# Kernel tuning notes

Hardware: AMD Instinct MI355X
Metric: run time of the kernel (lower is better)

The kernel has to match this reference:

```python
import jax, jax.numpy as jnp
import numpy as np

B, T, I, H, O = 4096, 2048, 1, 2, 1

def setup_inputs() -> dict:
    key = jax.random.key(0)
    ks = jax.random.split(key, 7)
    s_ih = 1.0 / np.sqrt(H)
    return {
        "x": jax.random.normal(ks[0], (B, T, I), dtype=jnp.float32),
        "W_ih": jax.random.uniform(ks[1], (H, I), jnp.float32, -s_ih, s_ih),
        "W_hh": jax.random.uniform(ks[2], (H, H), jnp.float32, -s_ih, s_ih),
        "b_ih": jax.random.uniform(ks[3], (H,), jnp.float32, -s_ih, s_ih),
        "b_hh": jax.random.uniform(ks[4], (H,), jnp.float32, -s_ih, s_ih),
        "fc_w": jax.random.uniform(ks[5], (O, H + I), jnp.float32, -1.0/np.sqrt(H + I), 1.0/np.sqrt(H + I)),
        "fc_b": jax.random.uniform(ks[6], (O,), jnp.float32, -1.0/np.sqrt(H + I), 1.0/np.sqrt(H + I)),
    }

def reference(x, W_ih, W_hh, b_ih, b_hh, fc_w, fc_b):
    # Precompute input contribution for all timesteps: [B, T, H]
    xin = jnp.einsum('bti,hi->bth', x, W_ih) + b_ih + b_hh
    h0 = jnp.zeros((x.shape[0], W_hh.shape[0]), dtype=x.dtype)

    def step(h, xin_t):  # h: [B,H], xin_t: [B,H]
        h_new = jnp.tanh(xin_t + h @ W_hh.T)
        return h_new, h_new

    _, hen = jax.lax.scan(step, h0, jnp.swapaxes(xin, 0, 1))  # hen: [T,B,H]
    hen = jnp.swapaxes(hen, 0, 1)  # [B,T,H]
    cat = jnp.concatenate((x, hen), axis=2)  # [B,T,I+H]
    return jnp.einsum('btc,oc->bto', cat, fc_w) + fc_b
```

## Files before the change

kernel.cpp:

```cpp
#include <hip/hip_runtime.h>


typedef float f32x2 __attribute__((ext_vector_type(2)));
typedef float f32x4 __attribute__((ext_vector_type(4)));

constexpr int T_LEN   = 2048;
constexpr int CHUNK   = 32;
constexpr int WARM    = 32;
constexpr int WPB     = 4;
constexpr int THREADS = 256;
constexpr int OSPAN   = WPB * CHUNK;
constexpr int SPAN    = OSPAN + WARM;
constexpr int NCG     = T_LEN / OSPAN;

static __device__ inline float EXP2F(float x){ float r; asm("v_exp_f32 %0, %1":"=v"(r):"v"(x)); return r; }
static __device__ inline float RCPF(float x){ float r; asm("v_rcp_f32 %0, %1":"=v"(r):"v"(x)); return r; }
static __device__ inline f32x2 mk2(float a, float b){ f32x2 t; t.x=a; t.y=b; return t; }

#define PK_FMA_B0(d, s0, s1, s2)                                          \
    asm("v_pk_fma_f32 %0, %1, %2, %3 op_sel:[0,0,0] op_sel_hi:[0,1,1]"    \
        : "=v"(d) : "v"(s0), "v"(s1), "v"(s2))
#define PK_FMA_B1(d, s0, s1, s2)                                          \
    asm("v_pk_fma_f32 %0, %1, %2, %3 op_sel:[1,0,0] op_sel_hi:[1,1,1]"    \
        : "=v"(d) : "v"(s0), "v"(s1), "v"(s2))
#define PK_ADD(d, s0, s1)                                                 \
    asm("v_pk_add_f32 %0, %1, %2" : "=v"(d) : "v"(s0), "v"(s1))

#define PSTEP_CORE(bb)                                                    \
    do {                                                                  \
        f32x2 q_, p_, e_, d_;                                             \
        PK_FMA_B1(q_, rr, mm1, (bb));                                     \
        PK_FMA_B0(p_, rr, mm0, q_);                                       \
        e_.x = EXP2F(p_.x); e_.y = EXP2F(p_.y);                           \
        PK_ADD(d_, e_, ones);                                             \
        rr.x = RCPF(d_.x); rr.y = RCPF(d_.y);                             \
    } while (0)

#define WSTEP_LO(xp2) do { f32x2 b_; PK_FMA_B0(b_, (xp2), aa, cc); PSTEP_CORE(b_); } while (0)
#define WSTEP_HI(xp2) do { f32x2 b_; PK_FMA_B1(b_, (xp2), aa, cc); PSTEP_CORE(b_); } while (0)
#define OSTEP_LO(xp2, ok) do { WSTEP_LO(xp2); (ok) = fmaf(rr.y, g2, fmaf(rr.x, g1, fmaf((xp2).x, f0, fb))); } while (0)
#define OSTEP_HI(xp2, ok) do { WSTEP_HI(xp2); (ok) = fmaf(rr.y, g2, fmaf(rr.x, g1, fmaf((xp2).y, f0, fb))); } while (0)

__global__ __launch_bounds__(THREADS, 4) void rnn_pk(
    const float* __restrict__ x,
    const float* __restrict__ W_ih,
    const float* __restrict__ W_hh,
    const float* __restrict__ b_ih,
    const float* __restrict__ b_hh,
    const float* __restrict__ fc_w,
    const float* __restrict__ fc_b,
    float* __restrict__ out)
{
    __shared__ float lx[SPAN * 64];

    const int sg  = blockIdx.x >> 4;
    const int cg  = blockIdx.x & (NCG - 1);
    const int tid = threadIdx.x;

    const int tlo = cg ? cg * OSPAN - WARM : 0;
    const float* xg = x + (size_t)sg * 64 * T_LEN + tlo;

    if (cg != 0) {
        #pragma unroll
        for (int k = 0; k < 10; ++k) {
            int idx = k * THREADS + tid;
            int r = idx / 40, c = idx - r * 40;
            f32x4 v = *(const f32x4*)(xg + (size_t)r * T_LEN + c * 4);
            int A = c * 256 + (((r ^ c) & 63) << 1);
            *(f32x2*)&lx[A]       = mk2(v.x, v.y);
            *(f32x2*)&lx[A + 128] = mk2(v.z, v.w);
        }
    } else {
        #pragma unroll
        for (int k = 0; k < 8; ++k) {
            int idx = k * THREADS + tid;
            int r = idx >> 5, c = idx & 31;
            f32x4 v = *(const f32x4*)(xg + (size_t)r * T_LEN + c * 4);
            int A = c * 256 + (((r ^ c) & 63) << 1);
            *(f32x2*)&lx[A]       = mk2(v.x, v.y);
            *(f32x2*)&lx[A + 128] = mk2(v.z, v.w);
        }
    }
    __syncthreads();

    const float s = 2.0f * 1.44269504088896340736f;
    const float W00 = W_hh[0], W01 = W_hh[1], W10 = W_hh[2], W11 = W_hh[3];
    const f32x2 aa  = mk2(W_ih[0] * s, W_ih[1] * s);
    const f32x2 cc  = mk2((b_ih[0] + b_hh[0] + W00 + W01) * s,
                          (b_ih[1] + b_hh[1] + W10 + W11) * s);
    const f32x2 mm0 = mk2(-2.0f * s * W00, -2.0f * s * W10);
    const f32x2 mm1 = mk2(-2.0f * s * W01, -2.0f * s * W11);
    const f32x2 ones = mk2(1.0f, 1.0f);
    const float f0 = fc_w[0];
    const float g1 = -2.0f * fc_w[1], g2 = -2.0f * fc_w[2];
    const float fb = fc_b[0] + fc_w[1] + fc_w[2];

    const int w = tid >> 6, l = tid & 63;

    int q, warm_q;
    if (cg == 0) {
        int gt = w * CHUNK - WARM;
        if (gt < 0) gt = 0;
        q = gt >> 2;
        warm_q = (w * CHUNK - gt) >> 2;
    } else {
        q = (w * CHUNK) >> 2;
        warm_q = WARM >> 2;
    }

    f32x2 rr = mk2(0.5f, 0.5f);

    #pragma unroll 2
    for (int i = 0; i < warm_q; ++i, ++q) {
        int A = q * 256 + (((l ^ q) & 63) << 1);
        f32x2 xa = *(const f32x2*)&lx[A];
        f32x2 xb = *(const f32x2*)&lx[A + 128];
        WSTEP_LO(xa); WSTEP_HI(xa); WSTEP_LO(xb); WSTEP_HI(xb);
    }

    f32x4 o0, o1, o2, o3, o4, o5, o6, o7;
#define OQ(oo)                                                            \
    do {                                                                  \
        int A = q * 256 + (((l ^ q) & 63) << 1);                          \
        f32x2 xa = *(const f32x2*)&lx[A];                                 \
        f32x2 xb = *(const f32x2*)&lx[A + 128];                           \
        OSTEP_LO(xa, oo.x); OSTEP_HI(xa, oo.y);                           \
        OSTEP_LO(xb, oo.z); OSTEP_HI(xb, oo.w);                           \
        ++q;                                                              \
    } while (0)
    OQ(o0); OQ(o1); OQ(o2); OQ(o3); OQ(o4); OQ(o5); OQ(o6); OQ(o7);

    __syncthreads();
#define OWR(oo, j)                                                        \
    do {                                                                  \
        int qo = w * 8 + (j);                                             \
        int A = qo * 256 + (((l ^ qo) & 63) << 1);                        \
        *(f32x2*)&lx[A]       = mk2((oo).x, (oo).y);                      \
        *(f32x2*)&lx[A + 128] = mk2((oo).z, (oo).w);                      \
    } while (0)
    OWR(o0, 0); OWR(o1, 1); OWR(o2, 2); OWR(o3, 3);
    OWR(o4, 4); OWR(o5, 5); OWR(o6, 6); OWR(o7, 7);
    __syncthreads();

    float* og = out + (size_t)sg * 64 * T_LEN + cg * OSPAN;
    #pragma unroll
    for (int k = 0; k < 8; ++k) {
        int idx = k * THREADS + tid;
        int r = idx >> 5, c = idx & 31;
        int A = c * 256 + (((r ^ c) & 63) << 1);
        f32x2 lo = *(const f32x2*)&lx[A];
        f32x2 hi = *(const f32x2*)&lx[A + 128];
        f32x4 v;
        v.x = lo.x; v.y = lo.y; v.z = hi.x; v.w = hi.y;
        __builtin_nontemporal_store(v, (f32x4*)(og + (size_t)r * T_LEN + c * 4));
    }
}

extern "C" void kernel_launch(void* const* d_in, const int* in_sizes, int n_in,
                              void* d_out, int out_size, void* d_ws, size_t ws_size,
                              hipStream_t stream) {
    const float* x    = (const float*)d_in[0];
    const float* W_ih = (const float*)d_in[1];
    const float* W_hh = (const float*)d_in[2];
    const float* b_ih = (const float*)d_in[3];
    const float* b_hh = (const float*)d_in[4];
    const float* fc_w = (const float*)d_in[5];
    const float* fc_b = (const float*)d_in[6];
    float* out = (float*)d_out;

    const int B = in_sizes[0] / T_LEN;

    dim3 block(THREADS);
    dim3 grid((B / 64) * NCG);
    rnn_pk<<<grid, block, 0, stream>>>(x, W_ih, W_hh, b_ih, b_hh,
                                       fc_w, fc_b, out);
}
```

Before: 19.13 us.

## Switch to one-wavefront blocks, each owning a 32-step chunk, removing barriers

Each block is now a single 64-lane wavefront that handles one 32-timestep chunk for 64 sequences, loading its own warm-up window and staging output through LDS. The three __syncthreads calls go away, since one wavefront needs no block barrier, and the grid becomes 4096 small blocks instead of 512 four-wave blocks. In exchange, every chunk after the first now reloads its 32-step warm-up input, whereas before the four waves in a block shared overlapping input. Each block also reserves 16 KB of LDS for a single wave, which may limit how many waves fit per CU.

```diff
diff --git a/kernel.cpp b/kernel.cpp
--- a/kernel.cpp
+++ b/kernel.cpp
@@ -4,14 +4,10 @@
 typedef float f32x2 __attribute__((ext_vector_type(2)));
 typedef float f32x4 __attribute__((ext_vector_type(4)));
 
-constexpr int T_LEN   = 2048;
-constexpr int CHUNK   = 32;
-constexpr int WARM    = 32;
-constexpr int WPB     = 4;
-constexpr int THREADS = 256;
-constexpr int OSPAN   = WPB * CHUNK;
-constexpr int SPAN    = OSPAN + WARM;
-constexpr int NCG     = T_LEN / OSPAN;
+constexpr int T_LEN  = 2048;
+constexpr int CHUNK  = 32;
+constexpr int WARM   = 32;
+constexpr int NCHUNK = T_LEN / CHUNK;
 
 static __device__ inline float EXP2F(float x){ float r; asm("v_exp_f32 %0, %1":"=v"(r):"v"(x)); return r; }
 static __device__ inline float RCPF(float x){ float r; asm("v_rcp_f32 %0, %1":"=v"(r):"v"(x)); return r; }
@@ -41,7 +37,7 @@
 #define OSTEP_LO(xp2, ok) do { WSTEP_LO(xp2); (ok) = fmaf(rr.y, g2, fmaf(rr.x, g1, fmaf((xp2).x, f0, fb))); } while (0)
 #define OSTEP_HI(xp2, ok) do { WSTEP_HI(xp2); (ok) = fmaf(rr.y, g2, fmaf(rr.x, g1, fmaf((xp2).y, f0, fb))); } while (0)
 
-__global__ __launch_bounds__(THREADS, 4) void rnn_pk(
+__global__ __launch_bounds__(64) void rnn_wave(
     const float* __restrict__ x,
     const float* __restrict__ W_ih,
     const float* __restrict__ W_hh,
@@ -51,108 +47,98 @@
     const float* __restrict__ fc_b,
     float* __restrict__ out)
 {
-    __shared__ float lx[SPAN * 64];
+    __shared__ float lx[4096];
 
-    const int sg  = blockIdx.x >> 4;
-    const int cg  = blockIdx.x & (NCG - 1);
-    const int tid = threadIdx.x;
+    const int l   = threadIdx.x;
+    const int wid = blockIdx.x;
+    const int sg  = wid >> 6;
+    const int c   = wid & (NCHUNK - 1);
 
-    const int tlo = cg ? cg * OSPAN - WARM : 0;
-    const float* xg = x + (size_t)sg * 64 * T_LEN + tlo;
+    const int t0 = c ? c * CHUNK - WARM : 0;
+    const int q0 = c ? (WARM >> 2) : 0;
 
-    if (cg != 0) {
+    const float* xg = x + (size_t)(sg * 64) * T_LEN + t0;
+
+    if (c) {
         #pragma unroll
-        for (int k = 0; k < 10; ++k) {
-            int idx = k * THREADS + tid;
-            int r = idx / 40, c = idx - r * 40;
-            f32x4 v = *(const f32x4*)(xg + (size_t)r * T_LEN + c * 4);
-            int A = c * 256 + (((r ^ c) & 63) << 1);
+        for (int k = 0; k < 16; ++k) {
+            int s = (l >> 4) + (k << 2);
+            int q = l & 15;
+            f32x4 v = *(const f32x4*)(xg + (size_t)s * T_LEN + (q << 2));
+            int A = q * 256 + (((s ^ q) & 63) << 1);
             *(f32x2*)&lx[A]       = mk2(v.x, v.y);
             *(f32x2*)&lx[A + 128] = mk2(v.z, v.w);
         }
     } else {
         #pragma unroll
         for (int k = 0; k < 8; ++k) {
-            int idx = k * THREADS + tid;
-            int r = idx >> 5, c = idx & 31;
-            f32x4 v = *(const f32x4*)(xg + (size_t)r * T_LEN + c * 4);
-            int A = c * 256 + (((r ^ c) & 63) << 1);
+            int s = (l >> 3) + (k << 3);
+            int q = l & 7;
+            f32x4 v = *(const f32x4*)(xg + (size_t)s * T_LEN + (q << 2));
+            int A = q * 256 + (((s ^ q) & 63) << 1);
             *(f32x2*)&lx[A]       = mk2(v.x, v.y);
             *(f32x2*)&lx[A + 128] = mk2(v.z, v.w);
         }
     }
-    __syncthreads();
 
-    const float s = 2.0f * 1.44269504088896340736f;
+    const float s2 = 2.0f * 1.44269504088896340736f;
     const float W00 = W_hh[0], W01 = W_hh[1], W10 = W_hh[2], W11 = W_hh[3];
-    const f32x2 aa  = mk2(W_ih[0] * s, W_ih[1] * s);
-    const f32x2 cc  = mk2((b_ih[0] + b_hh[0] + W00 + W01) * s,
-                          (b_ih[1] + b_hh[1] + W10 + W11) * s);
-    const f32x2 mm0 = mk2(-2.0f * s * W00, -2.0f * s * W10);
-    const f32x2 mm1 = mk2(-2.0f * s * W01, -2.0f * s * W11);
+    const f32x2 aa  = mk2(W_ih[0] * s2, W_ih[1] * s2);
+    const f32x2 cc  = mk2((b_ih[0] + b_hh[0] + W00 + W01) * s2,
+                          (b_ih[1] + b_hh[1] + W10 + W11) * s2);
+    const f32x2 mm0 = mk2(-2.0f * s2 * W00, -2.0f * s2 * W10);
+    const f32x2 mm1 = mk2(-2.0f * s2 * W01, -2.0f * s2 * W11);
     const f32x2 ones = mk2(1.0f, 1.0f);
     const float f0 = fc_w[0];
     const float g1 = -2.0f * fc_w[1], g2 = -2.0f * fc_w[2];
     const float fb = fc_b[0] + fc_w[1] + fc_w[2];
 
-    const int w = tid >> 6, l = tid & 63;
-
-    int q, warm_q;
-    if (cg == 0) {
-        int gt = w * CHUNK - WARM;
-        if (gt < 0) gt = 0;
-        q = gt >> 2;
-        warm_q = (w * CHUNK - gt) >> 2;
-    } else {
-        q = (w * CHUNK) >> 2;
-        warm_q = WARM >> 2;
-    }
-
     f32x2 rr = mk2(0.5f, 0.5f);
 
-    #pragma unroll 2
-    for (int i = 0; i < warm_q; ++i, ++q) {
-        int A = q * 256 + (((l ^ q) & 63) << 1);
-        f32x2 xa = *(const f32x2*)&lx[A];
-        f32x2 xb = *(const f32x2*)&lx[A + 128];
-        WSTEP_LO(xa); WSTEP_HI(xa); WSTEP_LO(xb); WSTEP_HI(xb);
+    if (c) {
+        #pragma unroll
+        for (int q = 0; q < 8; ++q) {
+            int A = q * 256 + (((l ^ q) & 63) << 1);
+            f32x2 xa = *(const f32x2*)&lx[A];
+            f32x2 xb = *(const f32x2*)&lx[A + 128];
+            WSTEP_LO(xa); WSTEP_HI(xa); WSTEP_LO(xb); WSTEP_HI(xb);
+        }
     }
 
     f32x4 o0, o1, o2, o3, o4, o5, o6, o7;
-#define OQ(oo)                                                            \
+#define OQ(oo, j)                                                         \
     do {                                                                  \
+        int q = q0 + (j);                                                 \
         int A = q * 256 + (((l ^ q) & 63) << 1);                          \
         f32x2 xa = *(const f32x2*)&lx[A];                                 \
         f32x2 xb = *(const f32x2*)&lx[A + 128];                           \
         OSTEP_LO(xa, oo.x); OSTEP_HI(xa, oo.y);                           \
         OSTEP_LO(xb, oo.z); OSTEP_HI(xb, oo.w);                           \
-        ++q;                                                              \
     } while (0)
-    OQ(o0); OQ(o1); OQ(o2); OQ(o3); OQ(o4); OQ(o5); OQ(o6); OQ(o7);
+    OQ(o0, 0); OQ(o1, 1); OQ(o2, 2); OQ(o3, 3);
+    OQ(o4, 4); OQ(o5, 5); OQ(o6, 6); OQ(o7, 7);
 
-    __syncthreads();
 #define OWR(oo, j)                                                        \
     do {                                                                  \
-        int qo = w * 8 + (j);                                             \
-        int A = qo * 256 + (((l ^ qo) & 63) << 1);                        \
+        int q = q0 + (j);                                                 \
+        int A = q * 256 + (((l ^ q) & 63) << 1);                          \
         *(f32x2*)&lx[A]       = mk2((oo).x, (oo).y);                      \
         *(f32x2*)&lx[A + 128] = mk2((oo).z, (oo).w);                      \
     } while (0)
     OWR(o0, 0); OWR(o1, 1); OWR(o2, 2); OWR(o3, 3);
     OWR(o4, 4); OWR(o5, 5); OWR(o6, 6); OWR(o7, 7);
-    __syncthreads();
 
-    float* og = out + (size_t)sg * 64 * T_LEN + cg * OSPAN;
+    float* og = out + (size_t)(sg * 64) * T_LEN + c * CHUNK;
     #pragma unroll
     for (int k = 0; k < 8; ++k) {
-        int idx = k * THREADS + tid;
-        int r = idx >> 5, c = idx & 31;
-        int A = c * 256 + (((r ^ c) & 63) << 1);
+        int s = (l >> 3) + (k << 3);
+        int j = l & 7;
+        int q = q0 + j;
+        int A = q * 256 + (((s ^ q) & 63) << 1);
         f32x2 lo = *(const f32x2*)&lx[A];
         f32x2 hi = *(const f32x2*)&lx[A + 128];
-        f32x4 v;
-        v.x = lo.x; v.y = lo.y; v.z = hi.x; v.w = hi.y;
-        __builtin_nontemporal_store(v, (f32x4*)(og + (size_t)r * T_LEN + c * 4));
+        f32x4 v; v.x = lo.x; v.y = lo.y; v.z = hi.x; v.w = hi.y;
+        __builtin_nontemporal_store(v, (f32x4*)(og + (size_t)s * T_LEN + (j << 2)));
     }
 }
 
@@ -170,8 +156,8 @@
 
     const int B = in_sizes[0] / T_LEN;
 
-    dim3 block(THREADS);
-    dim3 grid((B / 64) * NCG);
-    rnn_pk<<<grid, block, 0, stream>>>(x, W_ih, W_hh, b_ih, b_hh,
-                                       fc_w, fc_b, out);
+    dim3 block(64);
+    dim3 grid(B);
+    rnn_wave<<<grid, block, 0, stream>>>(x, W_ih, W_hh, b_ih, b_hh,
+                                         fc_w, fc_b, out);
 }
```

New measurement: 26.08 us. 1.36x slower.

## Process two time chunks per block with register prefetch of next chunk

Applied to the files above, without the earlier changes.

Each block now handles two consecutive time-chunk groups instead of one, halving the grid. While the first chunk's recurrence runs, the second chunk's x tile is loaded into registers, so its global load latency overlaps compute. A separate LDS output buffer lets the input tile be rewritten while outputs are staged. In exchange, launch bounds drop to 2 blocks per CU and there are half as many blocks, which reduces parallelism and increases register and LDS pressure.

```diff
diff --git a/kernel.cpp b/kernel.cpp
--- a/kernel.cpp
+++ b/kernel.cpp
@@ -12,6 +12,7 @@
 constexpr int OSPAN   = WPB * CHUNK;
 constexpr int SPAN    = OSPAN + WARM;
 constexpr int NCG     = T_LEN / OSPAN;
+constexpr int XQ      = SPAN / 4;
 
 static __device__ inline float EXP2F(float x){ float r; asm("v_exp_f32 %0, %1":"=v"(r):"v"(x)); return r; }
 static __device__ inline float RCPF(float x){ float r; asm("v_rcp_f32 %0, %1":"=v"(r):"v"(x)); return r; }
@@ -41,7 +42,77 @@
 #define OSTEP_LO(xp2, ok) do { WSTEP_LO(xp2); (ok) = fmaf(rr.y, g2, fmaf(rr.x, g1, fmaf((xp2).x, f0, fb))); } while (0)
 #define OSTEP_HI(xp2, ok) do { WSTEP_HI(xp2); (ok) = fmaf(rr.y, g2, fmaf(rr.x, g1, fmaf((xp2).y, f0, fb))); } while (0)
 
-__global__ __launch_bounds__(THREADS, 4) void rnn_pk(
+#define LOADX(dst, xgp)                                                   \
+    do {                                                                  \
+        _Pragma("unroll")                                                 \
+        for (int k = 0; k < 10; ++k) {                                    \
+            int idx = k * THREADS + tid;                                  \
+            int r_ = idx / XQ, c_ = idx - r_ * XQ;                        \
+            dst[k] = *(const f32x4*)((xgp) + (size_t)r_ * T_LEN + c_ * 4);\
+        }                                                                 \
+    } while (0)
+
+#define WRITEX(src)                                                       \
+    do {                                                                  \
+        _Pragma("unroll")                                                 \
+        for (int k = 0; k < 10; ++k) {                                    \
+            int idx = k * THREADS + tid;                                  \
+            int r_ = idx / XQ, c_ = idx - r_ * XQ;                        \
+            int A_ = c_ * 256 + (((r_ ^ c_) & 63) << 1);                  \
+            *(f32x2*)&lx[A_]       = mk2(src[k].x, src[k].y);             \
+            *(f32x2*)&lx[A_ + 128] = mk2(src[k].z, src[k].w);             \
+        }                                                                 \
+    } while (0)
+
+#define COMPUTE_OWR(cg)                                                   \
+    do {                                                                  \
+        int q, warm_q;                                                    \
+        if ((cg) == 0) {                                                  \
+            int gt = w * CHUNK - WARM; if (gt < 0) gt = 0;                \
+            q = gt >> 2; warm_q = (w * CHUNK - gt) >> 2;                  \
+        } else {                                                          \
+            q = (w * CHUNK) >> 2; warm_q = WARM >> 2;                     \
+        }                                                                 \
+        f32x2 rr = mk2(0.5f, 0.5f);                                       \
+        _Pragma("unroll 2")                                               \
+        for (int i = 0; i < warm_q; ++i, ++q) {                           \
+            int A_ = q * 256 + (((l ^ q) & 63) << 1);                     \
+            f32x2 xa_ = *(const f32x2*)&lx[A_];                           \
+            f32x2 xb_ = *(const f32x2*)&lx[A_ + 128];                     \
+            WSTEP_LO(xa_); WSTEP_HI(xa_); WSTEP_LO(xb_); WSTEP_HI(xb_);   \
+        }                                                                 \
+        _Pragma("unroll")                                                 \
+        for (int j = 0; j < 8; ++j, ++q) {                                \
+            int A_ = q * 256 + (((l ^ q) & 63) << 1);                     \
+            f32x2 xa_ = *(const f32x2*)&lx[A_];                           \
+            f32x2 xb_ = *(const f32x2*)&lx[A_ + 128];                     \
+            f32x4 oo;                                                     \
+            OSTEP_LO(xa_, oo.x); OSTEP_HI(xa_, oo.y);                     \
+            OSTEP_LO(xb_, oo.z); OSTEP_HI(xb_, oo.w);                     \
+            int qo = w * 8 + j;                                           \
+            int Ao = qo * 256 + (((l ^ qo) & 63) << 1);                   \
+            *(f32x2*)&lo_buf[Ao]       = mk2(oo.x, oo.y);                 \
+            *(f32x2*)&lo_buf[Ao + 128] = mk2(oo.z, oo.w);                 \
+        }                                                                 \
+    } while (0)
+
+#define STOREO(cg)                                                        \
+    do {                                                                  \
+        float* og = out + (size_t)(sg * 64) * T_LEN + (cg) * OSPAN;       \
+        _Pragma("unroll")                                                 \
+        for (int k = 0; k < 8; ++k) {                                     \
+            int idx = k * THREADS + tid;                                  \
+            int r_ = idx >> 5, c_ = idx & 31;                             \
+            int A_ = c_ * 256 + (((r_ ^ c_) & 63) << 1);                  \
+            f32x2 lo_ = *(const f32x2*)&lo_buf[A_];                       \
+            f32x2 hi_ = *(const f32x2*)&lo_buf[A_ + 128];                 \
+            f32x4 v_; v_.x = lo_.x; v_.y = lo_.y; v_.z = hi_.x; v_.w = hi_.y; \
+            __builtin_nontemporal_store(v_,                               \
+                (f32x4*)(og + (size_t)r_ * T_LEN + c_ * 4));              \
+        }                                                                 \
+    } while (0)
+
+__global__ __launch_bounds__(THREADS, 2) void rnn_pipe(
     const float* __restrict__ x,
     const float* __restrict__ W_ih,
     const float* __restrict__ W_hh,
@@ -52,108 +123,46 @@
     float* __restrict__ out)
 {
     __shared__ float lx[SPAN * 64];
+    __shared__ float lo_buf[OSPAN * 64];
 
-    const int sg  = blockIdx.x >> 4;
-    const int cg  = blockIdx.x & (NCG - 1);
+    const int sg  = blockIdx.x >> 3;
+    const int bcg = blockIdx.x & 7;
+    const int cgA = bcg * 2, cgB = bcg * 2 + 1;
     const int tid = threadIdx.x;
+    const int w = tid >> 6, l = tid & 63;
 
-    const int tlo = cg ? cg * OSPAN - WARM : 0;
-    const float* xg = x + (size_t)sg * 64 * T_LEN + tlo;
+    const float* xbase = x + (size_t)(sg * 64) * T_LEN;
+    const int tloA = cgA ? cgA * OSPAN - WARM : 0;
+    const int tloB = cgB * OSPAN - WARM;
 
-    if (cg != 0) {
-        #pragma unroll
-        for (int k = 0; k < 10; ++k) {
-            int idx = k * THREADS + tid;
-            int r = idx / 40, c = idx - r * 40;
-            f32x4 v = *(const f32x4*)(xg + (size_t)r * T_LEN + c * 4);
-            int A = c * 256 + (((r ^ c) & 63) << 1);
-            *(f32x2*)&lx[A]       = mk2(v.x, v.y);
-            *(f32x2*)&lx[A + 128] = mk2(v.z, v.w);
-        }
-    } else {
-        #pragma unroll
-        for (int k = 0; k < 8; ++k) {
-            int idx = k * THREADS + tid;
-            int r = idx >> 5, c = idx & 31;
-            f32x4 v = *(const f32x4*)(xg + (size_t)r * T_LEN + c * 4);
-            int A = c * 256 + (((r ^ c) & 63) << 1);
-            *(f32x2*)&lx[A]       = mk2(v.x, v.y);
-            *(f32x2*)&lx[A + 128] = mk2(v.z, v.w);
-        }
-    }
-    __syncthreads();
-
-    const float s = 2.0f * 1.44269504088896340736f;
+    const float s2 = 2.0f * 1.44269504088896340736f;
     const float W00 = W_hh[0], W01 = W_hh[1], W10 = W_hh[2], W11 = W_hh[3];
-    const f32x2 aa  = mk2(W_ih[0] * s, W_ih[1] * s);
-    const f32x2 cc  = mk2((b_ih[0] + b_hh[0] + W00 + W01) * s,
-                          (b_ih[1] + b_hh[1] + W10 + W11) * s);
-    const f32x2 mm0 = mk2(-2.0f * s * W00, -2.0f * s * W10);
-    const f32x2 mm1 = mk2(-2.0f * s * W01, -2.0f * s * W11);
+    const f32x2 aa  = mk2(W_ih[0] * s2, W_ih[1] * s2);
+    const f32x2 cc  = mk2((b_ih[0] + b_hh[0] + W00 + W01) * s2,
+                          (b_ih[1] + b_hh[1] + W10 + W11) * s2);
+    const f32x2 mm0 = mk2(-2.0f * s2 * W00, -2.0f * s2 * W10);
+    const f32x2 mm1 = mk2(-2.0f * s2 * W01, -2.0f * s2 * W11);
     const f32x2 ones = mk2(1.0f, 1.0f);
     const float f0 = fc_w[0];
     const float g1 = -2.0f * fc_w[1], g2 = -2.0f * fc_w[2];
     const float fb = fc_b[0] + fc_w[1] + fc_w[2];
 
-    const int w = tid >> 6, l = tid & 63;
+    f32x4 rbuf[10];
 
-    int q, warm_q;
-    if (cg == 0) {
-        int gt = w * CHUNK - WARM;
-        if (gt < 0) gt = 0;
-        q = gt >> 2;
-        warm_q = (w * CHUNK - gt) >> 2;
-    } else {
-        q = (w * CHUNK) >> 2;
-        warm_q = WARM >> 2;
-    }
-
-    f32x2 rr = mk2(0.5f, 0.5f);
-
-    #pragma unroll 2
-    for (int i = 0; i < warm_q; ++i, ++q) {
-        int A = q * 256 + (((l ^ q) & 63) << 1);
-        f32x2 xa = *(const f32x2*)&lx[A];
-        f32x2 xb = *(const f32x2*)&lx[A + 128];
-        WSTEP_LO(xa); WSTEP_HI(xa); WSTEP_LO(xb); WSTEP_HI(xb);
-    }
-
-    f32x4 o0, o1, o2, o3, o4, o5, o6, o7;
-#define OQ(oo)                                                            \
-    do {                                                                  \
-        int A = q * 256 + (((l ^ q) & 63) << 1);                          \
-        f32x2 xa = *(const f32x2*)&lx[A];                                 \
-        f32x2 xb = *(const f32x2*)&lx[A + 128];                           \
-        OSTEP_LO(xa, oo.x); OSTEP_HI(xa, oo.y);                           \
-        OSTEP_LO(xb, oo.z); OSTEP_HI(xb, oo.w);                           \
-        ++q;                                                              \
-    } while (0)
-    OQ(o0); OQ(o1); OQ(o2); OQ(o3); OQ(o4); OQ(o5); OQ(o6); OQ(o7);
-
-    __syncthreads();
-#define OWR(oo, j)                                                        \
-    do {                                                                  \
-        int qo = w * 8 + (j);                                             \
-        int A = qo * 256 + (((l ^ qo) & 63) << 1);                        \
-        *(f32x2*)&lx[A]       = mk2((oo).x, (oo).y);                      \
-        *(f32x2*)&lx[A + 128] = mk2((oo).z, (oo).w);                      \
-    } while (0)
-    OWR(o0, 0); OWR(o1, 1); OWR(o2, 2); OWR(o3, 3);
-    OWR(o4, 4); OWR(o5, 5); OWR(o6, 6); OWR(o7, 7);
+    LOADX(rbuf, xbase + tloA);
+    WRITEX(rbuf);
     __syncthreads();
 
-    float* og = out + (size_t)sg * 64 * T_LEN + cg * OSPAN;
-    #pragma unroll
-    for (int k = 0; k < 8; ++k) {
-        int idx = k * THREADS + tid;
-        int r = idx >> 5, c = idx & 31;
-        int A = c * 256 + (((r ^ c) & 63) << 1);
-        f32x2 lo = *(const f32x2*)&lx[A];
-        f32x2 hi = *(const f32x2*)&lx[A + 128];
-        f32x4 v;
-        v.x = lo.x; v.y = lo.y; v.z = hi.x; v.w = hi.y;
-        __builtin_nontemporal_store(v, (f32x4*)(og + (size_t)r * T_LEN + c * 4));
-    }
+    LOADX(rbuf, xbase + tloB);
+    COMPUTE_OWR(cgA);
+    __syncthreads();
+    WRITEX(rbuf);
+    STOREO(cgA);
+    __syncthreads();
+
+    COMPUTE_OWR(cgB);
+    __syncthreads();
+    STOREO(cgB);
 }
 
 extern "C" void kernel_launch(void* const* d_in, const int* in_sizes, int n_in,
@@ -171,7 +180,7 @@
     const int B = in_sizes[0] / T_LEN;
 
     dim3 block(THREADS);
-    dim3 grid((B / 64) * NCG);
-    rnn_pk<<<grid, block, 0, stream>>>(x, W_ih, W_hh, b_ih, b_hh,
-                                       fc_w, fc_b, out);
+    dim3 grid((B / 64) * (NCG / 2));
+    rnn_pipe<<<grid, block, 0, stream>>>(x, W_ih, W_hh, b_ih, b_hh,
+                                         fc_w, fc_b, out);
 }
```

New measurement: 20.49 us. 7.1% more time.

## Shrink blocks to two waves, drop load barrier with per-wave staging, remap grid

Applied to the files above, without the earlier changes.

Blocks go from four waves to two, each covering 64 timesteps, which doubles the grid. Each wave now loads exactly the shared-memory columns its own recurrence reads, so the barrier after the load is removed. The outputs are written back into the wave's own staging region, leaving a single barrier before the store. The block index is permuted to interleave chunk groups across blocks. The cost is more redundant warm-up work per output timestep (32 warm steps per 64 outputs instead of per 128), in exchange for less synchronization and finer scheduling granularity.

```diff
diff --git a/kernel.cpp b/kernel.cpp
--- a/kernel.cpp
+++ b/kernel.cpp
@@ -7,9 +7,8 @@
 constexpr int T_LEN   = 2048;
 constexpr int CHUNK   = 32;
 constexpr int WARM    = 32;
-constexpr int WPB     = 4;
-constexpr int THREADS = 256;
-constexpr int OSPAN   = WPB * CHUNK;
+constexpr int THREADS = 128;
+constexpr int OSPAN   = 64;
 constexpr int SPAN    = OSPAN + WARM;
 constexpr int NCG     = T_LEN / OSPAN;
 
@@ -41,7 +40,17 @@
 #define OSTEP_LO(xp2, ok) do { WSTEP_LO(xp2); (ok) = fmaf(rr.y, g2, fmaf(rr.x, g1, fmaf((xp2).x, f0, fb))); } while (0)
 #define OSTEP_HI(xp2, ok) do { WSTEP_HI(xp2); (ok) = fmaf(rr.y, g2, fmaf(rr.x, g1, fmaf((xp2).y, f0, fb))); } while (0)
 
-__global__ __launch_bounds__(THREADS, 4) void rnn_pk(
+#define OQ(oo)                                                            \
+    do {                                                                  \
+        int A_ = q * 256 + (((l ^ q) & 63) << 1);                         \
+        f32x2 xa_ = *(const f32x2*)&lx[A_];                               \
+        f32x2 xb_ = *(const f32x2*)&lx[A_ + 128];                         \
+        OSTEP_LO(xa_, oo.x); OSTEP_HI(xa_, oo.y);                         \
+        OSTEP_LO(xb_, oo.z); OSTEP_HI(xb_, oo.w);                         \
+        ++q;                                                              \
+    } while (0)
+
+__global__ __launch_bounds__(THREADS, 3) void rnn_w2(
     const float* __restrict__ x,
     const float* __restrict__ W_ih,
     const float* __restrict__ W_hh,
@@ -53,106 +62,94 @@
 {
     __shared__ float lx[SPAN * 64];
 
-    const int sg  = blockIdx.x >> 4;
-    const int cg  = blockIdx.x & (NCG - 1);
+    const int lb  = ((blockIdx.x & 7) << 8) + (blockIdx.x >> 3);
+    const int sg  = lb >> 5;
+    const int cg  = lb & (NCG - 1);
     const int tid = threadIdx.x;
+    const int w   = tid >> 6, l = tid & 63;
 
     const int tlo = cg ? cg * OSPAN - WARM : 0;
-    const float* xg = x + (size_t)sg * 64 * T_LEN + tlo;
+    const float* xg = x + (size_t)(sg * 64) * T_LEN + tlo;
 
-    if (cg != 0) {
+    if (cg == 0 && w == 0) {
         #pragma unroll
-        for (int k = 0; k < 10; ++k) {
-            int idx = k * THREADS + tid;
-            int r = idx / 40, c = idx - r * 40;
-            f32x4 v = *(const f32x4*)(xg + (size_t)r * T_LEN + c * 4);
-            int A = c * 256 + (((r ^ c) & 63) << 1);
-            *(f32x2*)&lx[A]       = mk2(v.x, v.y);
-            *(f32x2*)&lx[A + 128] = mk2(v.z, v.w);
+        for (int k = 0; k < 8; ++k) {
+            int r_ = (k << 3) + (l >> 3), c_ = l & 7;
+            f32x4 v = *(const f32x4*)(xg + (size_t)r_ * T_LEN + (c_ << 2));
+            int A_ = c_ * 256 + (((r_ ^ c_) & 63) << 1);
+            *(f32x2*)&lx[A_]       = mk2(v.x, v.y);
+            *(f32x2*)&lx[A_ + 128] = mk2(v.z, v.w);
         }
     } else {
+        const int gb = cg ? w * 8 : 0;
         #pragma unroll
-        for (int k = 0; k < 8; ++k) {
-            int idx = k * THREADS + tid;
-            int r = idx >> 5, c = idx & 31;
-            f32x4 v = *(const f32x4*)(xg + (size_t)r * T_LEN + c * 4);
-            int A = c * 256 + (((r ^ c) & 63) << 1);
-            *(f32x2*)&lx[A]       = mk2(v.x, v.y);
-            *(f32x2*)&lx[A + 128] = mk2(v.z, v.w);
+        for (int k = 0; k < 16; ++k) {
+            int r_ = (k << 2) + (l >> 4), c_ = gb + (l & 15);
+            f32x4 v = *(const f32x4*)(xg + (size_t)r_ * T_LEN + (c_ << 2));
+            int A_ = c_ * 256 + (((r_ ^ c_) & 63) << 1);
+            *(f32x2*)&lx[A_]       = mk2(v.x, v.y);
+            *(f32x2*)&lx[A_ + 128] = mk2(v.z, v.w);
         }
     }
-    __syncthreads();
 
-    const float s = 2.0f * 1.44269504088896340736f;
+    const float s2 = 2.0f * 1.44269504088896340736f;
     const float W00 = W_hh[0], W01 = W_hh[1], W10 = W_hh[2], W11 = W_hh[3];
-    const f32x2 aa  = mk2(W_ih[0] * s, W_ih[1] * s);
-    const f32x2 cc  = mk2((b_ih[0] + b_hh[0] + W00 + W01) * s,
-                          (b_ih[1] + b_hh[1] + W10 + W11) * s);
-    const f32x2 mm0 = mk2(-2.0f * s * W00, -2.0f * s * W10);
-    const f32x2 mm1 = mk2(-2.0f * s * W01, -2.0f * s * W11);
+    const f32x2 aa  = mk2(W_ih[0] * s2, W_ih[1] * s2);
+    const f32x2 cc  = mk2((b_ih[0] + b_hh[0] + W00 + W01) * s2,
+                          (b_ih[1] + b_hh[1] + W10 + W11) * s2);
+    const f32x2 mm0 = mk2(-2.0f * s2 * W00, -2.0f * s2 * W10);
+    const f32x2 mm1 = mk2(-2.0f * s2 * W01, -2.0f * s2 * W11);
     const f32x2 ones = mk2(1.0f, 1.0f);
     const float f0 = fc_w[0];
     const float g1 = -2.0f * fc_w[1], g2 = -2.0f * fc_w[2];
     const float fb = fc_b[0] + fc_w[1] + fc_w[2];
 
-    const int w = tid >> 6, l = tid & 63;
-
-    int q, warm_q;
-    if (cg == 0) {
-        int gt = w * CHUNK - WARM;
-        if (gt < 0) gt = 0;
-        q = gt >> 2;
-        warm_q = (w * CHUNK - gt) >> 2;
-    } else {
-        q = (w * CHUNK) >> 2;
-        warm_q = WARM >> 2;
+    f32x4 o0, o1, o2, o3, o4, o5, o6, o7;
+    {
+        int q, warm_q;
+        if (cg == 0) {
+            int gt = w * CHUNK - WARM; if (gt < 0) gt = 0;
+            q = gt >> 2; warm_q = (w * CHUNK - gt) >> 2;
+        } else {
+            q = w * 8; warm_q = 8;
+        }
+        f32x2 rr = mk2(0.5f, 0.5f);
+        #pragma unroll 2
+        for (int i = 0; i < warm_q; ++i, ++q) {
+            int A_ = q * 256 + (((l ^ q) & 63) << 1);
+            f32x2 xa_ = *(const f32x2*)&lx[A_];
+            f32x2 xb_ = *(const f32x2*)&lx[A_ + 128];
+            WSTEP_LO(xa_); WSTEP_HI(xa_); WSTEP_LO(xb_); WSTEP_HI(xb_);
+        }
+        OQ(o0); OQ(o1); OQ(o2); OQ(o3); OQ(o4); OQ(o5); OQ(o6); OQ(o7);
     }
 
-    f32x2 rr = mk2(0.5f, 0.5f);
-
-    #pragma unroll 2
-    for (int i = 0; i < warm_q; ++i, ++q) {
-        int A = q * 256 + (((l ^ q) & 63) << 1);
-        f32x2 xa = *(const f32x2*)&lx[A];
-        f32x2 xb = *(const f32x2*)&lx[A + 128];
-        WSTEP_LO(xa); WSTEP_HI(xa); WSTEP_LO(xb); WSTEP_HI(xb);
-    }
-
-    f32x4 o0, o1, o2, o3, o4, o5, o6, o7;
-#define OQ(oo)                                                            \
-    do {                                                                  \
-        int A = q * 256 + (((l ^ q) & 63) << 1);                          \
-        f32x2 xa = *(const f32x2*)&lx[A];                                 \
-        f32x2 xb = *(const f32x2*)&lx[A + 128];                           \
-        OSTEP_LO(xa, oo.x); OSTEP_HI(xa, oo.y);                           \
-        OSTEP_LO(xb, oo.z); OSTEP_HI(xb, oo.w);                           \
-        ++q;                                                              \
-    } while (0)
-    OQ(o0); OQ(o1); OQ(o2); OQ(o3); OQ(o4); OQ(o5); OQ(o6); OQ(o7);
-
-    __syncthreads();
-#define OWR(oo, j)                                                        \
-    do {                                                                  \
-        int qo = w * 8 + (j);                                             \
-        int A = qo * 256 + (((l ^ qo) & 63) << 1);                        \
-        *(f32x2*)&lx[A]       = mk2((oo).x, (oo).y);                      \
-        *(f32x2*)&lx[A + 128] = mk2((oo).z, (oo).w);                      \
-    } while (0)
-    OWR(o0, 0); OWR(o1, 1); OWR(o2, 2); OWR(o3, 3);
-    OWR(o4, 4); OWR(o5, 5); OWR(o6, 6); OWR(o7, 7);
     __syncthreads();
 
-    float* og = out + (size_t)sg * 64 * T_LEN + cg * OSPAN;
+    const int qb = cg ? w * 8 : (w == 0 ? 16 : 8);
+    #pragma unroll
+    for (int j = 0; j < 8; ++j) {
+        f32x4 oo = (j==0)?o0:(j==1)?o1:(j==2)?o2:(j==3)?o3:
+                   (j==4)?o4:(j==5)?o5:(j==6)?o6:o7;
+        int qo = qb + j;
+        int Ao = qo * 256 + (((l ^ qo) & 63) << 1);
+        *(f32x2*)&lx[Ao]       = mk2(oo.x, oo.y);
+        *(f32x2*)&lx[Ao + 128] = mk2(oo.z, oo.w);
+    }
+    float* og = out + (size_t)(sg * 64) * T_LEN + cg * OSPAN;
     #pragma unroll
     for (int k = 0; k < 8; ++k) {
-        int idx = k * THREADS + tid;
-        int r = idx >> 5, c = idx & 31;
-        int A = c * 256 + (((r ^ c) & 63) << 1);
-        f32x2 lo = *(const f32x2*)&lx[A];
-        f32x2 hi = *(const f32x2*)&lx[A + 128];
-        f32x4 v;
-        v.x = lo.x; v.y = lo.y; v.z = hi.x; v.w = hi.y;
-        __builtin_nontemporal_store(v, (f32x4*)(og + (size_t)r * T_LEN + c * 4));
+        int idx = k * 64 + l;
+        int r_ = idx >> 3;
+        int jj = idx & 7;
+        int qg = qb + jj;
+        int c_ = w * 8 + jj;
+        int A_ = qg * 256 + (((r_ ^ qg) & 63) << 1);
+        f32x2 lo_ = *(const f32x2*)&lx[A_];
+        f32x2 hi_ = *(const f32x2*)&lx[A_ + 128];
+        f32x4 v_; v_.x = lo_.x; v_.y = lo_.y; v_.z = hi_.x; v_.w = hi_.y;
+        __builtin_nontemporal_store(v_,
+            (f32x4*)(og + (size_t)r_ * T_LEN + (c_ << 2)));
     }
 }
 
@@ -172,6 +169,6 @@
 
     dim3 block(THREADS);
     dim3 grid((B / 64) * NCG);
-    rnn_pk<<<grid, block, 0, stream>>>(x, W_ih, W_hh, b_ih, b_hh,
+    rnn_w2<<<grid, block, 0, stream>>>(x, W_ih, W_hh, b_ih, b_hh,
                                        fc_w, fc_b, out);
 }
```

Result: slower. 21.12 us (+10.4%).
